# Performance work log

Measured on AMD Instinct MI355X. Metric: run time of the kernel, lower is better.

The kernel has to match this reference:

```python
import jax, jax.numpy as jnp
import numpy as np

N_TERMS = 2048  # zonotope error terms (x[0] center + 2047 generators)
N = 4096        # neurons


def setup_inputs() -> dict:
    key = jax.random.key(0)
    x = jax.random.normal(key, (N_TERMS, N), dtype=jnp.float32)
    return {"x": x}


def reference(x):
    n_terms, n = x.shape
    # interval bounds of the zonotope
    abs_sum = jnp.sum(jnp.abs(x[1:]), axis=0)      # [n]
    upper = x[0] + abs_sum
    lower = x[0] - abs_sum

    cross = (lower * upper) < 0                    # neuron straddles 0
    pos = lower >= 0                               # strictly non-negative
    crossf = cross.astype(x.dtype)
    posf = pos.astype(x.dtype)

    # 'auto' lambda init: upper/(upper-lower) on crossing neurons, 1 on positive,
    # NaN (0/0) replaced by 0.5; lambda is set via .data => constant w.r.t. x.
    denom = upper - lower
    safe = denom != 0
    lam = posf + crossf * jnp.where(safe, upper / jnp.where(safe, denom, 1.0), 0.5)
    lam = jax.lax.stop_gradient(lam)

    delta = jnp.maximum(-lam * lower, (1.0 - lam) * upper)  # [n]

    center = (delta * 0.5 + lam * x[0]) * crossf + x[0] * posf
    gens = x[1:] * (lam * crossf + posf)                    # [n_terms-1, n]

    # Parallel stream-compaction: crossing neuron i gets its own new error row
    # at n_terms + (# crossings before i). Padded to worst case n new rows;
    # non-crossing writes land on distinct (row, col) slots with value 0.
    ci = cross.astype(jnp.int32)
    rows = n_terms + jnp.cumsum(ci) - ci               # exclusive prefix sum
    cols = jnp.arange(n)

    out = jnp.zeros((n_terms + n, n), x.dtype)
    out = out.at[0].set(center)
    out = out.at[1:n_terms].set(gens)
    out = out.at[rows, cols].add((delta * 0.5) * crossf)
    return out
```

## Files before the change

kernel.cpp:

```cpp
#include <hip/hip_runtime.h>

#define N_TERMS 2048
#define NCOL 4096
#define NC4 1024
#define NCHUNK 128
#define RPC (N_TERMS / NCHUNK)

typedef float f4_t __attribute__((ext_vector_type(4)));

__global__ void k_partial_abs(const float* __restrict__ x, float* __restrict__ partial,
                              int* __restrict__ done_ctr) {
    if (blockIdx.x == 0 && blockIdx.y == 0 && threadIdx.x == 0) *done_ctr = 0;
    int col4 = blockIdx.x * blockDim.x + threadIdx.x;
    int chunk = blockIdx.y;
    int r0 = chunk * RPC;
    int r1 = r0 + RPC;
    if (r0 == 0) r0 = 1;
    const f4_t* x4 = (const f4_t*)x;
    f4_t acc = {0.f, 0.f, 0.f, 0.f};
#pragma unroll
    for (int r = r0; r < r1; ++r) {
        f4_t v = x4[(long)r * NC4 + col4];
        acc.x += fabsf(v.x);
        acc.y += fabsf(v.y);
        acc.z += fabsf(v.z);
        acc.w += fabsf(v.w);
    }
    ((f4_t*)partial)[chunk * NC4 + col4] = acc;
}

__global__ void k_stats(const float* __restrict__ x, const float* __restrict__ partial,
                        float* __restrict__ out0, float* __restrict__ scale,
                        float* __restrict__ dhalf, int* __restrict__ crossflag,
                        int* __restrict__ rowtarget, int* __restrict__ done_ctr) {
    const int t = threadIdx.x;
    const int lane = t & 63;
    const int q = t >> 6;
    const int c = blockIdx.x * 64 + lane;

    float s0 = 0.f, s1 = 0.f, s2 = 0.f, s3 = 0.f;
    const int k0 = q * 32;
#pragma unroll 8
    for (int k = 0; k < 32; k += 4) {
        s0 += partial[(k0 + k + 0) * NCOL + c];
        s1 += partial[(k0 + k + 1) * NCOL + c];
        s2 += partial[(k0 + k + 2) * NCOL + c];
        s3 += partial[(k0 + k + 3) * NCOL + c];
    }
    __shared__ float red[4][64];
    red[q][lane] = (s0 + s1) + (s2 + s3);
    __syncthreads();
    if (q == 0) {
        float s = (red[0][lane] + red[1][lane]) + (red[2][lane] + red[3][lane]);
        float x0 = x[c];
        float u = x0 + s;
        float l = x0 - s;
        bool cross = (l * u) < 0.0f;
        bool pos = (l >= 0.0f);
        float denom = u - l;
        float lam = (pos ? 1.0f : 0.0f) +
                    (cross ? ((denom != 0.0f) ? u / denom : 0.5f) : 0.0f);
        float delta = fmaxf(-lam * l, (1.0f - lam) * u);
        float crossf = cross ? 1.0f : 0.0f;
        float posf = pos ? 1.0f : 0.0f;
        out0[c] = (delta * 0.5f + lam * x0) * crossf + x0 * posf;
        scale[c] = lam * crossf + posf;
        dhalf[c] = delta * 0.5f * crossf;
        crossflag[c] = cross ? 1 : 0;
    }

    __threadfence();
    __shared__ int is_last;
    if (t == 0) is_last = (atomicAdd(done_ctr, 1) == (int)gridDim.x - 1);
    __syncthreads();
    if (!is_last) return;
    __threadfence();

    const int T = 256;
    const int PER = NCOL / T;
    __shared__ int tsum[T];
    const int base = t * PER;
    int ex[PER];
    int run = 0;
#pragma unroll
    for (int i = 0; i < PER; ++i) {
        ex[i] = run;
        run += crossflag[base + i];
    }
    tsum[t] = run;
    __syncthreads();
    for (int off = 1; off < T; off <<= 1) {
        int v = 0;
        if (t >= off) v = tsum[t - off];
        __syncthreads();
        tsum[t] += v;
        __syncthreads();
    }
    int excl = (t == 0) ? 0 : tsum[t - 1];
#pragma unroll
    for (int i = 0; i < PER; ++i) rowtarget[base + i] = N_TERMS + excl + ex[i];
}

__global__ void k_write(const float* __restrict__ x, const float* __restrict__ scale,
                        const float* __restrict__ dhalf, const int* __restrict__ rowtarget,
                        float* __restrict__ out) {
    long g = (long)blockIdx.x * blockDim.x + threadIdx.x;
    int col4 = (int)(g & 1023);
    int group = (int)(g >> 10);
    int r0 = group << 2;
    const f4_t* x4 = (const f4_t*)x;
    f4_t* o4 = (f4_t*)out;

    if (group < 512) {
        f4_t sc = ((const f4_t*)scale)[col4];
        if (group == 0) {
#pragma unroll
            for (int r = 1; r < 4; ++r) {
                f4_t v = x4[(long)r * NC4 + col4] * sc;
                __builtin_nontemporal_store(v, &o4[(long)r * NC4 + col4]);
            }
        } else {
#pragma unroll
            for (int i = 0; i < 4; ++i) {
                int r = r0 + i;
                f4_t v = x4[(long)r * NC4 + col4] * sc;
                __builtin_nontemporal_store(v, &o4[(long)r * NC4 + col4]);
            }
        }
    } else {
        int4 rt = ((const int4*)rowtarget)[col4];
        f4_t dh = ((const f4_t*)dhalf)[col4];
#pragma unroll
        for (int i = 0; i < 4; ++i) {
            int r = r0 + i;
            f4_t v;
            v.x = (rt.x == r) ? dh.x : 0.0f;
            v.y = (rt.y == r) ? dh.y : 0.0f;
            v.z = (rt.z == r) ? dh.z : 0.0f;
            v.w = (rt.w == r) ? dh.w : 0.0f;
            __builtin_nontemporal_store(v, &o4[(long)r * NC4 + col4]);
        }
    }
}

extern "C" void kernel_launch(void* const* d_in, const int* in_sizes, int n_in,
                              void* d_out, int out_size, void* d_ws, size_t ws_size,
                              hipStream_t stream) {
    const float* x = (const float*)d_in[0];
    float* out = (float*)d_out;

    float* ws = (float*)d_ws;
    float* partial   = ws;
    float* scale     = partial + NCHUNK * NCOL;
    float* dhalf     = scale + NCOL;
    int*   crossflag = (int*)(dhalf + NCOL);
    int*   rowtarget = crossflag + NCOL;
    int*   done_ctr  = rowtarget + NCOL;

    k_partial_abs<<<dim3(NC4 / 256, NCHUNK), 256, 0, stream>>>(x, partial, done_ctr);
    k_stats<<<64, 256, 0, stream>>>(x, partial, out, scale, dhalf, crossflag,
                                    rowtarget, done_ctr);

    const int blocks = 1536 * 1024 / 256;
    k_write<<<blocks, 256, 0, stream>>>(x, scale, dhalf, rowtarget, out);
}
```

Measured before the change: 140.9 us.

## Move zero-fill into the reduction pass and scatter deltas from stats kernel

The zero padding region of the output is now written by extra blocks in the first (abs-sum reduction) kernel instead of after the stats kernel, so those stores no longer wait on the scan. The last stats block scatters the delta values directly into their compacted rows, which removes the rowtarget buffer and the compare-select writes. The final kernel only writes the scaled generator rows. The risk is that the serialized scatter in one block adds latency to the stats kernel.

```diff
diff --git a/kernel.cpp b/kernel.cpp
--- a/kernel.cpp
+++ b/kernel.cpp
@@ -8,31 +8,43 @@
 
 typedef float f4_t __attribute__((ext_vector_type(4)));
 
-__global__ void k_partial_abs(const float* __restrict__ x, float* __restrict__ partial,
-                              int* __restrict__ done_ctr) {
-    if (blockIdx.x == 0 && blockIdx.y == 0 && threadIdx.x == 0) *done_ctr = 0;
-    int col4 = blockIdx.x * blockDim.x + threadIdx.x;
-    int chunk = blockIdx.y;
-    int r0 = chunk * RPC;
-    int r1 = r0 + RPC;
-    if (r0 == 0) r0 = 1;
-    const f4_t* x4 = (const f4_t*)x;
-    f4_t acc = {0.f, 0.f, 0.f, 0.f};
+__global__ void k_pass1(const float* __restrict__ x, float* __restrict__ partial,
+                        float* __restrict__ out, int* __restrict__ done_ctr) {
+    const int b = blockIdx.x;
+    const int t = threadIdx.x;
+    if (b < 512) {
+        if (b == 0 && t == 0) *done_ctr = 0;
+        const int col4 = (b & 3) * 256 + t;
+        const int chunk = b >> 2;
+        int r0 = chunk * RPC;
+        const int r1 = r0 + RPC;
+        if (r0 == 0) r0 = 1;
+        const f4_t* x4 = (const f4_t*)x;
+        f4_t acc = {0.f, 0.f, 0.f, 0.f};
 #pragma unroll
-    for (int r = r0; r < r1; ++r) {
-        f4_t v = x4[(long)r * NC4 + col4];
-        acc.x += fabsf(v.x);
-        acc.y += fabsf(v.y);
-        acc.z += fabsf(v.z);
-        acc.w += fabsf(v.w);
+        for (int r = r0; r < r1; ++r) {
+            f4_t v = x4[(long)r * NC4 + col4];
+            acc.x += fabsf(v.x);
+            acc.y += fabsf(v.y);
+            acc.z += fabsf(v.z);
+            acc.w += fabsf(v.w);
+        }
+        ((f4_t*)partial)[chunk * NC4 + col4] = acc;
+    } else {
+        const int zb = b - 512;
+        f4_t* o4 = (f4_t*)out;
+        const long base4 = (long)N_TERMS * NC4 + (long)zb * 2048;
+        const f4_t z = {0.f, 0.f, 0.f, 0.f};
+#pragma unroll
+        for (int i = 0; i < 8; ++i)
+            __builtin_nontemporal_store(z, &o4[base4 + i * 256 + t]);
     }
-    ((f4_t*)partial)[chunk * NC4 + col4] = acc;
 }
 
 __global__ void k_stats(const float* __restrict__ x, const float* __restrict__ partial,
-                        float* __restrict__ out0, float* __restrict__ scale,
+                        float* __restrict__ out, float* __restrict__ scale,
                         float* __restrict__ dhalf, int* __restrict__ crossflag,
-                        int* __restrict__ rowtarget, int* __restrict__ done_ctr) {
+                        int* __restrict__ done_ctr) {
     const int t = threadIdx.x;
     const int lane = t & 63;
     const int q = t >> 6;
@@ -63,7 +75,7 @@
         float delta = fmaxf(-lam * l, (1.0f - lam) * u);
         float crossf = cross ? 1.0f : 0.0f;
         float posf = pos ? 1.0f : 0.0f;
-        out0[c] = (delta * 0.5f + lam * x0) * crossf + x0 * posf;
+        out[c] = (delta * 0.5f + lam * x0) * crossf + x0 * posf;
         scale[c] = lam * crossf + posf;
         dhalf[c] = delta * 0.5f * crossf;
         crossflag[c] = cross ? 1 : 0;
@@ -80,12 +92,14 @@
     const int PER = NCOL / T;
     __shared__ int tsum[T];
     const int base = t * PER;
+    int cf[PER];
     int ex[PER];
     int run = 0;
 #pragma unroll
     for (int i = 0; i < PER; ++i) {
+        cf[i] = crossflag[base + i];
         ex[i] = run;
-        run += crossflag[base + i];
+        run += cf[i];
     }
     tsum[t] = run;
     __syncthreads();
@@ -96,48 +110,38 @@
         tsum[t] += v;
         __syncthreads();
     }
-    int excl = (t == 0) ? 0 : tsum[t - 1];
+    const int excl = (t == 0) ? 0 : tsum[t - 1];
 #pragma unroll
-    for (int i = 0; i < PER; ++i) rowtarget[base + i] = N_TERMS + excl + ex[i];
+    for (int i = 0; i < PER; ++i) {
+        if (cf[i]) {
+            const int c2 = base + i;
+            const long row = N_TERMS + excl + ex[i];
+            out[row * (long)NCOL + c2] = dhalf[c2];
+        }
+    }
 }
 
-__global__ void k_write(const float* __restrict__ x, const float* __restrict__ scale,
-                        const float* __restrict__ dhalf, const int* __restrict__ rowtarget,
-                        float* __restrict__ out) {
-    long g = (long)blockIdx.x * blockDim.x + threadIdx.x;
-    int col4 = (int)(g & 1023);
-    int group = (int)(g >> 10);
-    int r0 = group << 2;
+__global__ void k_gens(const float* __restrict__ x, const float* __restrict__ scale,
+                       float* __restrict__ out) {
+    const int g = blockIdx.x * blockDim.x + threadIdx.x;
+    const int col4 = g & 1023;
+    const int group = g >> 10;
+    const int r0 = group << 2;
     const f4_t* x4 = (const f4_t*)x;
     f4_t* o4 = (f4_t*)out;
+    const f4_t sc = ((const f4_t*)scale)[col4];
 
-    if (group < 512) {
-        f4_t sc = ((const f4_t*)scale)[col4];
-        if (group == 0) {
+    if (group == 0) {
 #pragma unroll
-            for (int r = 1; r < 4; ++r) {
-                f4_t v = x4[(long)r * NC4 + col4] * sc;
-                __builtin_nontemporal_store(v, &o4[(long)r * NC4 + col4]);
-            }
-        } else {
-#pragma unroll
-            for (int i = 0; i < 4; ++i) {
-                int r = r0 + i;
-                f4_t v = x4[(long)r * NC4 + col4] * sc;
-                __builtin_nontemporal_store(v, &o4[(long)r * NC4 + col4]);
-            }
+        for (int r = 1; r < 4; ++r) {
+            f4_t v = x4[(long)r * NC4 + col4] * sc;
+            __builtin_nontemporal_store(v, &o4[(long)r * NC4 + col4]);
         }
     } else {
-        int4 rt = ((const int4*)rowtarget)[col4];
-        f4_t dh = ((const f4_t*)dhalf)[col4];
 #pragma unroll
         for (int i = 0; i < 4; ++i) {
-            int r = r0 + i;
-            f4_t v;
-            v.x = (rt.x == r) ? dh.x : 0.0f;
-            v.y = (rt.y == r) ? dh.y : 0.0f;
-            v.z = (rt.z == r) ? dh.z : 0.0f;
-            v.w = (rt.w == r) ? dh.w : 0.0f;
+            const int r = r0 + i;
+            f4_t v = x4[(long)r * NC4 + col4] * sc;
             __builtin_nontemporal_store(v, &o4[(long)r * NC4 + col4]);
         }
     }
@@ -154,13 +158,9 @@
     float* scale     = partial + NCHUNK * NCOL;
     float* dhalf     = scale + NCOL;
     int*   crossflag = (int*)(dhalf + NCOL);
-    int*   rowtarget = crossflag + NCOL;
-    int*   done_ctr  = rowtarget + NCOL;
+    int*   done_ctr  = crossflag + NCOL;
 
-    k_partial_abs<<<dim3(NC4 / 256, NCHUNK), 256, 0, stream>>>(x, partial, done_ctr);
-    k_stats<<<64, 256, 0, stream>>>(x, partial, out, scale, dhalf, crossflag,
-                                    rowtarget, done_ctr);
-
-    const int blocks = 1536 * 1024 / 256;
-    k_write<<<blocks, 256, 0, stream>>>(x, scale, dhalf, rowtarget, out);
+    k_pass1<<<2560, 256, 0, stream>>>(x, partial, out, done_ctr);
+    k_stats<<<64, 256, 0, stream>>>(x, partial, out, scale, dhalf, crossflag, done_ctr);
+    k_gens<<<2048, 256, 0, stream>>>(x, scale, out);
 }
```

Result: slower. 146.5 us (+4.0%).
